# Kernel tuning notes

Measured on AMD Instinct MI355X. Metric: run time of the kernel, lower is better.

## Reference

```python
import jax, jax.numpy as jnp
import numpy as np

HIDDEN_DIM = 4096
NUM_SHARDS = 64
TOP_K = 2
B = 16384


def setup_inputs() -> dict:
    key = jax.random.key(0)
    k_h, k_w = jax.random.split(key)
    h = jax.random.normal(k_h, (B, HIDDEN_DIM), dtype=jnp.float32)
    # nn.init.normal_(weight, std=0.02); bias zeros
    weight = jax.random.normal(k_w, (NUM_SHARDS, HIDDEN_DIM), dtype=jnp.float32) * 0.02
    bias = jnp.zeros((NUM_SHARDS,), dtype=jnp.float32)
    return {"h": h, "weight": weight, "bias": bias}


def reference(h, weight, bias):
    # logits: (B, num_shards)
    logits = jnp.einsum("bd,ed->be", h, weight) + bias
    probs = jax.nn.softmax(logits, axis=-1)
    k = min(TOP_K, weight.shape[0])
    topk_vals, topk_idx = jax.lax.top_k(probs, k)
    denom = jnp.maximum(jnp.sum(topk_vals, axis=-1, keepdims=True), 1e-12)
    topk_w = topk_vals / denom
    return topk_w, topk_idx
```

## Files before the change

kernel.cpp:

```cpp
#include <hip/hip_runtime.h>
#include <math.h>


#define HIDDEN   4096
#define NSHARD   64
#define B_ROWS   16384
#define WGT      256
#define ROWS_WG  16
#define KC       128
#define NCHUNK   (HIDDEN / KC)
#define KCP      132
#define LDSF     (4 * 16 * KCP)

__global__ __launch_bounds__(WGT, 4)
void gate_kernel(const float* __restrict__ h,
                 const float* __restrict__ w,
                 const float* __restrict__ bias,
                 float* __restrict__ out)
{
    __shared__ float lw[LDSF];

    const int tid = threadIdx.x;
    const int g   = tid & 15;
    const int ks  = (tid >> 4) & 3;
    const int rg  = tid >> 6;
    const int row0 = blockIdx.x * ROWS_WG + rg * 4;

    const float* __restrict__ hbase = h + (size_t)row0 * HIDDEN;

    float acc[4][4];
#pragma unroll
    for (int r = 0; r < 4; ++r)
#pragma unroll
        for (int j = 0; j < 4; ++j) acc[r][j] = 0.0f;

    for (int c = 0; c < NCHUNK; ++c) {
        __syncthreads();
#pragma unroll
        for (int t = 0; t < 8; ++t) {
            const int idx = t * WGT + tid;
            const int kq  = idx & 31;
            const int e   = idx >> 5;
            const float4 v = *(const float4*)(w + (size_t)e * HIDDEN + c * KC + kq * 4);
            const int j  = e & 3;
            const int gg = e >> 2;
            *(float4*)(lw + j * (16 * KCP) + gg * KCP + kq * 4) = v;
        }
        __syncthreads();

#pragma unroll
        for (int step = 0; step < 8; ++step) {
            const int kin = c * KC + ks * 32 + step * 4;
            float4 hv[4];
#pragma unroll
            for (int r = 0; r < 4; ++r)
                hv[r] = *(const float4*)(hbase + (size_t)r * HIDDEN + kin);
#pragma unroll
            for (int j = 0; j < 4; ++j) {
                const float4 wv = *(const float4*)(lw + j * (16 * KCP) + g * KCP
                                                   + ks * 32 + step * 4);
#pragma unroll
                for (int r = 0; r < 4; ++r) {
                    acc[r][j] = fmaf(hv[r].x, wv.x, acc[r][j]);
                    acc[r][j] = fmaf(hv[r].y, wv.y, acc[r][j]);
                    acc[r][j] = fmaf(hv[r].z, wv.z, acc[r][j]);
                    acc[r][j] = fmaf(hv[r].w, wv.w, acc[r][j]);
                }
            }
        }
    }

#pragma unroll
    for (int m = 16; m <= 32; m <<= 1)
#pragma unroll
        for (int r = 0; r < 4; ++r)
#pragma unroll
            for (int j = 0; j < 4; ++j)
                acc[r][j] += __shfl_xor(acc[r][j], m, 64);

    const float4 bv = *(const float4*)(bias + g * 4);
    float m1[4], m2[4];
    int   i1[4], i2[4];
#pragma unroll
    for (int r = 0; r < 4; ++r) {
        float v0 = acc[r][0] + bv.x, v1 = acc[r][1] + bv.y;
        float v2 = acc[r][2] + bv.z, v3 = acc[r][3] + bv.w;
        float a1 = v0, a2 = -INFINITY; int b1 = g * 4, b2 = 0;
        if (v1 > a1)      { a2 = a1; b2 = b1; a1 = v1; b1 = g * 4 + 1; }
        else              { a2 = v1; b2 = g * 4 + 1; }
        if (v2 > a1)      { a2 = a1; b2 = b1; a1 = v2; b1 = g * 4 + 2; }
        else if (v2 > a2) { a2 = v2; b2 = g * 4 + 2; }
        if (v3 > a1)      { a2 = a1; b2 = b1; a1 = v3; b1 = g * 4 + 3; }
        else if (v3 > a2) { a2 = v3; b2 = g * 4 + 3; }
        m1[r] = a1; i1[r] = b1; m2[r] = a2; i2[r] = b2;
    }

#pragma unroll
    for (int m = 1; m <= 8; m <<= 1) {
#pragma unroll
        for (int r = 0; r < 4; ++r) {
            const float o1 = __shfl_xor(m1[r], m, 64);
            const int   q1 = __shfl_xor(i1[r], m, 64);
            const float o2 = __shfl_xor(m2[r], m, 64);
            const int   q2 = __shfl_xor(i2[r], m, 64);
            const bool take = (o1 > m1[r]) || (o1 == m1[r] && q1 < i1[r]);
            const float w1 = take ? o1 : m1[r]; const int w1i = take ? q1 : i1[r];
            const float l1 = take ? m1[r] : o1; const int l1i = take ? i1[r] : q1;
            const float s2 = take ? o2 : m2[r]; const int s2i = take ? q2 : i2[r];
            const bool t2 = (l1 > s2) || (l1 == s2 && l1i < s2i);
            m1[r] = w1; i1[r] = w1i;
            m2[r] = t2 ? l1 : s2; i2[r] = t2 ? l1i : s2i;
        }
    }

    if ((tid & 63) == 0) {
        float* __restrict__ oidx = out + 2 * B_ROWS;
#pragma unroll
        for (int r = 0; r < 4; ++r) {
            const int row = row0 + r;
            const float ed  = expf(m2[r] - m1[r]);
            const float inv = 1.0f / (1.0f + ed);
            out[2 * row + 0] = inv;
            out[2 * row + 1] = ed * inv;
            oidx[2 * row + 0] = (float)i1[r];
            oidx[2 * row + 1] = (float)i2[r];
        }
    }
}

extern "C" void kernel_launch(void* const* d_in, const int* in_sizes, int n_in,
                              void* d_out, int out_size, void* d_ws, size_t ws_size,
                              hipStream_t stream)
{
    const float* h    = (const float*)d_in[0];
    const float* wt   = (const float*)d_in[1];
    const float* bias = (const float*)d_in[2];
    float* out = (float*)d_out;

    gate_kernel<<<dim3(B_ROWS / ROWS_WG), dim3(WGT), 0, stream>>>(h, wt, bias, out);
}
```

Before: 529.7 us.

## Double rows per thread and XOR-swizzle LDS weight layout

Each thread now accumulates 8 rows instead of 4, so every LDS weight read feeds twice as many FMAs and each workgroup loads the weight tile for 32 rows instead of 16. The padded LDS layout is replaced with a float4 XOR-swizzled layout meant to avoid bank conflicts without padding. The cost is roughly double the accumulator and h-register footprint, which may lower occupancy under the launch bounds, and half as many workgroups are launched.

```diff
diff --git a/kernel.cpp b/kernel.cpp
--- a/kernel.cpp
+++ b/kernel.cpp
@@ -6,11 +6,10 @@
 #define NSHARD   64
 #define B_ROWS   16384
 #define WGT      256
-#define ROWS_WG  16
+#define ROWS_WG  32
+#define RPT      8
 #define KC       128
 #define NCHUNK   (HIDDEN / KC)
-#define KCP      132
-#define LDSF     (4 * 16 * KCP)
 
 __global__ __launch_bounds__(WGT, 4)
 void gate_kernel(const float* __restrict__ h,
@@ -18,19 +17,20 @@
                  const float* __restrict__ bias,
                  float* __restrict__ out)
 {
-    __shared__ float lw[LDSF];
+    __shared__ float4 lwq[2048];
 
     const int tid = threadIdx.x;
     const int g   = tid & 15;
     const int ks  = (tid >> 4) & 3;
     const int rg  = tid >> 6;
-    const int row0 = blockIdx.x * ROWS_WG + rg * 4;
+    const int row0 = blockIdx.x * ROWS_WG + rg * RPT;
 
     const float* __restrict__ hbase = h + (size_t)row0 * HIDDEN;
+    const float4* __restrict__ wq   = (const float4*)w;
 
-    float acc[4][4];
+    float acc[RPT][4];
 #pragma unroll
-    for (int r = 0; r < 4; ++r)
+    for (int r = 0; r < RPT; ++r)
 #pragma unroll
         for (int j = 0; j < 4; ++j) acc[r][j] = 0.0f;
 
@@ -39,28 +39,29 @@
 #pragma unroll
         for (int t = 0; t < 8; ++t) {
             const int idx = t * WGT + tid;
+            const int e   = idx >> 5;
             const int kq  = idx & 31;
-            const int e   = idx >> 5;
-            const float4 v = *(const float4*)(w + (size_t)e * HIDDEN + c * KC + kq * 4);
+            const float4 v = wq[(size_t)e * (HIDDEN / 4) + c * 32 + kq];
             const int j  = e & 3;
-            const int gg = e >> 2;
-            *(float4*)(lw + j * (16 * KCP) + gg * KCP + kq * 4) = v;
+            const int ge = e >> 2;
+            lwq[j * 512 + kq * 16 + (ge ^ (kq & 15))] = v;
         }
         __syncthreads();
 
 #pragma unroll
         for (int step = 0; step < 8; ++step) {
-            const int kin = c * KC + ks * 32 + step * 4;
-            float4 hv[4];
+            const int kq  = ks * 8 + step;
+            const int kin = c * KC + kq * 4;
+            float4 hv[RPT];
 #pragma unroll
-            for (int r = 0; r < 4; ++r)
+            for (int r = 0; r < RPT; ++r)
                 hv[r] = *(const float4*)(hbase + (size_t)r * HIDDEN + kin);
+            const int gx = g ^ (kq & 15);
 #pragma unroll
             for (int j = 0; j < 4; ++j) {
-                const float4 wv = *(const float4*)(lw + j * (16 * KCP) + g * KCP
-                                                   + ks * 32 + step * 4);
+                const float4 wv = lwq[j * 512 + kq * 16 + gx];
 #pragma unroll
-                for (int r = 0; r < 4; ++r) {
+                for (int r = 0; r < RPT; ++r) {
                     acc[r][j] = fmaf(hv[r].x, wv.x, acc[r][j]);
                     acc[r][j] = fmaf(hv[r].y, wv.y, acc[r][j]);
                     acc[r][j] = fmaf(hv[r].z, wv.z, acc[r][j]);
@@ -73,16 +74,16 @@
 #pragma unroll
     for (int m = 16; m <= 32; m <<= 1)
 #pragma unroll
-        for (int r = 0; r < 4; ++r)
+        for (int r = 0; r < RPT; ++r)
 #pragma unroll
             for (int j = 0; j < 4; ++j)
                 acc[r][j] += __shfl_xor(acc[r][j], m, 64);
 
     const float4 bv = *(const float4*)(bias + g * 4);
-    float m1[4], m2[4];
-    int   i1[4], i2[4];
+    float m1[RPT], m2[RPT];
+    int   i1[RPT], i2[RPT];
 #pragma unroll
-    for (int r = 0; r < 4; ++r) {
+    for (int r = 0; r < RPT; ++r) {
         float v0 = acc[r][0] + bv.x, v1 = acc[r][1] + bv.y;
         float v2 = acc[r][2] + bv.z, v3 = acc[r][3] + bv.w;
         float a1 = v0, a2 = -INFINITY; int b1 = g * 4, b2 = 0;
@@ -98,7 +99,7 @@
 #pragma unroll
     for (int m = 1; m <= 8; m <<= 1) {
 #pragma unroll
-        for (int r = 0; r < 4; ++r) {
+        for (int r = 0; r < RPT; ++r) {
             const float o1 = __shfl_xor(m1[r], m, 64);
             const int   q1 = __shfl_xor(i1[r], m, 64);
             const float o2 = __shfl_xor(m2[r], m, 64);
@@ -116,7 +117,7 @@
     if ((tid & 63) == 0) {
         float* __restrict__ oidx = out + 2 * B_ROWS;
 #pragma unroll
-        for (int r = 0; r < 4; ++r) {
+        for (int r = 0; r < RPT; ++r) {
             const int row = row0 + r;
             const float ed  = expf(m2[r] - m1[r]);
             const float inv = 1.0f / (1.0f + ed);
```

After: 584.3 us. 1.1x slower.
